# Performance work log

Hardware: AMD Instinct MI355X
Metric: run time of the kernel (lower is better)

The kernel has to match this reference:

```python
import jax, jax.numpy as jnp
import numpy as np

NEG_INF = -1e8  # masked_fill value from the torch code
EPS_DICE = 0.001
EPS_DIV = 1e-5
LOSS_FACTOR = 1.0  # loss['factor']


def conv2d(x, w, b, pad):
    # x: [B,C,H,W], w: [O,I,kh,kw] (OIHW), b: [O]
    y = jax.lax.conv_general_dilated(
        x, w, window_strides=(1, 1), padding=[(pad, pad), (pad, pad)],
        dimension_numbers=("NCHW", "OIHW", "NCHW"))
    return y + b[None, :, None, None]


def setup_inputs() -> dict:
    key = jax.random.key(0)
    ks = jax.random.split(key, 12)
    B, C, H, W = 2, 256, 64, 64
    s = 0.05  # small init scale to keep logits in a sane range
    inp = {
        "feats": jax.random.normal(ks[0], (B, C, H, W), jnp.float32),
        "masks": jax.random.randint(ks[1], (B, H, W), 0, 2).astype(jnp.float32),
        "layouts": jax.random.randint(ks[2], (B, H, W), 0, 16).astype(jnp.int32),
        "w_pre0": jax.random.normal(ks[3], (C, C, 3, 3), jnp.float32) * s,
        "b_pre0": jax.random.normal(ks[4], (C,), jnp.float32) * s,
        "w_pre1": jax.random.normal(ks[5], (C, C, 3, 3), jnp.float32) * s,
        "b_pre1": jax.random.normal(ks[6], (C,), jnp.float32) * s,
        "w_kernel": jax.random.normal(ks[7], (C + 1, C, 1, 1), jnp.float32) * s,
        "b_kernel": jax.random.normal(ks[8], (C + 1,), jnp.float32) * s,
        "w_feats": jax.random.normal(ks[9], (C, C, 1, 1), jnp.float32) * s,
        "b_feats": jax.random.normal(ks[10], (C,), jnp.float32) * s,
    }
    return inp


def reference(feats, masks, layouts, w_pre0, b_pre0, w_pre1, b_pre1,
              w_kernel, b_kernel, w_feats, b_feats):
    B, C, H, W = feats.shape
    # pre_kernel_convs: two 3x3 conv + ReLU
    h = jax.nn.relu(conv2d(feats, w_pre0, b_pre0, pad=1))
    h = jax.nn.relu(conv2d(h, w_pre1, b_pre1, pad=1))
    kernels = conv2d(h, w_kernel, b_kernel, pad=0)          # [B, C+1, H, W]
    f = conv2d(feats, w_feats, b_feats, pad=0)               # [B, C,   H, W]
    # permute(0,2,3,1).reshape(B, H*W, C+1): per-cell dynamic 1x1 conv params
    kernels = kernels.transpose(0, 2, 3, 1).reshape(B, H * W, C + 1)
    kw = kernels[..., :C]                                    # [B, P, C]
    kb = kernels[..., C]                                     # [B, P]
    # grouped 1x1 conv == batched matmul over channel dim
    logits = jnp.einsum("bpc,bchw->bphw", kw, f) + kb[:, :, None, None]
    logits = jnp.where(masks[:, None, :, :] > 0, logits, NEG_INF)  # [B,P,H,W]

    # --- training loss (dice, div='all') ---
    # segm_labels[b, r*W+c] = (layouts[b] == layouts[b,r,c])
    flat = layouts.reshape(B, H * W)
    labels = (layouts[:, None, :, :] == flat[:, :, None, None]).astype(logits.dtype)
    p = jax.nn.sigmoid(logits)
    d = 2.0 * (p * labels) / (p * p + EPS_DICE + labels * labels + EPS_DICE)
    loss_el = 1.0 - d                                        # [B, P, H, W]
    m_flat = masks.reshape(B, H * W)
    num = ((loss_el * masks[:, None, :, :]).sum((-1, -2)) * m_flat).sum(-1)  # [B]
    grid = masks.sum((1, 2))
    loss = (LOSS_FACTOR * num / (grid * grid + EPS_DIV)).mean()
    return logits, loss
```

## Files before the change

kernel.cpp:

```cpp
#include <hip/hip_runtime.h>
#include <hip/hip_bf16.h>
#include <math.h>

typedef __attribute__((ext_vector_type(8))) short bf16x8;
typedef __attribute__((ext_vector_type(4))) float f32x4;
typedef __hip_bfloat16 bf16_t;

#define NEG_INF_V -100000000.0f

__device__ __forceinline__ void gload16(const void* g, void* l) {
  __builtin_amdgcn_global_load_lds(
      (const __attribute__((address_space(1))) unsigned int*)g,
      (__attribute__((address_space(3))) unsigned int*)l, 16, 0, 0);
}

__device__ __forceinline__ bf16x8 swzread(const short* base, int r, int c) {
  return *(const bf16x8*)(base + ((r * 8 + (c ^ (r & 7))) << 3));
}

__global__ __launch_bounds__(256) void pad_cast_k(
    const float* __restrict__ feats, bf16_t* __restrict__ x_pad) {
  __shared__ float s[64][65];
  const int t = threadIdx.x;
  const int y = blockIdx.x, c0 = blockIdx.y * 64, b = blockIdx.z;
  const float* fb = feats + ((size_t)b * 256 + c0) * 4096 + y * 64;
  for (int i = t; i < 64 * 64; i += 256) {
    int ci = i >> 6, x = i & 63;
    s[ci][x] = fb[(size_t)ci * 4096 + x];
  }
  __syncthreads();
  bf16_t* xp = x_pad + (size_t)b * (66 * 66 * 256) + ((size_t)(y + 1) * 66 + 1) * 256 + c0;
  for (int i = t; i < 64 * 64; i += 256) {
    int x = i >> 6, ci = i & 63;
    xp[(size_t)x * 256 + ci] = __float2bfloat16(s[ci][x]);
  }
}

__global__ __launch_bounds__(256) void castw3_k(
    const float* __restrict__ w0, const float* __restrict__ w1,
    bf16_t* __restrict__ o0, bf16_t* __restrict__ o1) {
  const int co = blockIdx.x, t = threadIdx.x;
  const float* ws = blockIdx.y ? w1 : w0;
  bf16_t* wd = blockIdx.y ? o1 : o0;
#pragma unroll
  for (int k = 0; k < 9; ++k)
    wd[(size_t)co * 2304 + k * 256 + t] = __float2bfloat16(ws[((size_t)co * 256 + t) * 9 + k]);
}

__global__ __launch_bounds__(256) void castw1_k(
    const float* __restrict__ wk, const float* __restrict__ wf,
    bf16_t* __restrict__ ok, bf16_t* __restrict__ of) {
  int i = blockIdx.x * 256 + threadIdx.x;
  if (i < 257 * 256) ok[i] = __float2bfloat16(wk[i]);
  else { int j = i - 257 * 256; if (j < 256 * 256) of[j] = __float2bfloat16(wf[j]); }
}

__global__ __launch_bounds__(256) void conv3x3_mfma_k(
    const bf16_t* __restrict__ xpad, const bf16_t* __restrict__ wr,
    const float* __restrict__ bias, bf16_t* __restrict__ out,
    int out_row_stride, int out_base, long out_bstride) {
  __shared__ __align__(16) short ldsA[2][4096];
  __shared__ __align__(16) short ldsB[2][4096];
  const int t = threadIdx.x, w = t >> 6, lane = t & 63;
  const int y = blockIdx.x, co0 = blockIdx.y * 64, b = blockIdx.z;
  const bf16_t* xb = xpad + (size_t)b * (66 * 66 * 256);
  const int wm = w >> 1, wn = w & 1;
  f32x4 acc[2][2] = {};

  int ar[2], ac[2];
#pragma unroll
  for (int p = 0; p < 2; ++p) {
    int u = (p * 4 + w) * 64 + lane;
    ar[p] = u >> 3;
    ac[p] = ((u & 7) ^ ((u >> 3) & 7)) * 8;
  }
  const int fr = lane & 15, fc = lane >> 4;

  auto stage = [&](int ks, int buf) {
    int kpos = ks >> 2, cik = (ks & 3) * 64;
    int ky = (kpos * 11) >> 5, kx = kpos - 3 * ky;
#pragma unroll
    for (int p = 0; p < 2; ++p) {
      gload16(xb + ((size_t)(y + ky) * 66 + (ar[p] + kx)) * 256 + cik + ac[p],
              &ldsA[buf][(p * 4 + w) * 512]);
      gload16(wr + (size_t)(co0 + ar[p]) * 2304 + kpos * 256 + cik + ac[p],
              &ldsB[buf][(p * 4 + w) * 512]);
    }
  };
  auto compute = [&](int buf) {
#pragma unroll
    for (int kk = 0; kk < 2; ++kk) {
      bf16x8 af[2], bfr[2];
#pragma unroll
      for (int m = 0; m < 2; ++m) af[m] = swzread(ldsA[buf], wm * 32 + m * 16 + fr, kk * 4 + fc);
#pragma unroll
      for (int n = 0; n < 2; ++n) bfr[n] = swzread(ldsB[buf], wn * 32 + n * 16 + fr, kk * 4 + fc);
#pragma unroll
      for (int m = 0; m < 2; ++m)
#pragma unroll
        for (int n = 0; n < 2; ++n)
          acc[m][n] = __builtin_amdgcn_mfma_f32_16x16x32_bf16(af[m], bfr[n], acc[m][n], 0, 0, 0);
    }
  };

  stage(0, 0);
  __syncthreads();
  for (int ks = 0; ks < 35; ++ks) {
    stage(ks + 1, (ks + 1) & 1);
    compute(ks & 1);
    __syncthreads();
  }
  compute(1);

  bf16_t* ob = out + (size_t)b * out_bstride;
  float bv[2];
#pragma unroll
  for (int n = 0; n < 2; ++n) bv[n] = bias[co0 + wn * 32 + n * 16 + fr];
#pragma unroll
  for (int m = 0; m < 2; ++m)
#pragma unroll
    for (int r = 0; r < 4; ++r) {
      int x = wm * 32 + m * 16 + fc * 4 + r;
      size_t ra = (size_t)out_base + (size_t)y * out_row_stride + (size_t)x * 256 + co0 + wn * 32 + fr;
#pragma unroll
      for (int n = 0; n < 2; ++n) {
        float v = acc[m][n][r] + bv[n];
        ob[ra + n * 16] = __float2bfloat16(fmaxf(v, 0.f));
      }
    }
}

template <bool KER>
__global__ __launch_bounds__(256) void conv1x1_mfma_k(
    const bf16_t* __restrict__ in, const bf16_t* __restrict__ wt,
    const float* __restrict__ bias, bf16_t* __restrict__ outw,
    float* __restrict__ outkb, int A0, int AS, long in_bstride, int comax) {
  __shared__ __align__(16) short ldsA[2][4096];
  __shared__ __align__(16) short ldsB[2][4096];
  const int t = threadIdx.x, w = t >> 6, lane = t & 63;
  const int y = blockIdx.x, co0 = blockIdx.y * 64, b = blockIdx.z;
  const bf16_t* inb = in + (size_t)b * in_bstride;
  const int wm = w >> 1, wn = w & 1;
  f32x4 acc[2][2] = {};

  int ar[2], ac[2];
#pragma unroll
  for (int p = 0; p < 2; ++p) {
    int u = (p * 4 + w) * 64 + lane;
    ar[p] = u >> 3;
    ac[p] = ((u & 7) ^ ((u >> 3) & 7)) * 8;
  }
  const int fr = lane & 15, fc = lane >> 4;

  auto stage = [&](int ks, int buf) {
    int cik = ks * 64;
#pragma unroll
    for (int p = 0; p < 2; ++p) {
      gload16(inb + (size_t)A0 + (size_t)y * AS + (size_t)ar[p] * 256 + cik + ac[p],
              &ldsA[buf][(p * 4 + w) * 512]);
      gload16(wt + (size_t)min(co0 + ar[p], comax - 1) * 256 + cik + ac[p],
              &ldsB[buf][(p * 4 + w) * 512]);
    }
  };
  auto compute = [&](int buf) {
#pragma unroll
    for (int kk = 0; kk < 2; ++kk) {
      bf16x8 af[2], bfr[2];
#pragma unroll
      for (int m = 0; m < 2; ++m) af[m] = swzread(ldsA[buf], wm * 32 + m * 16 + fr, kk * 4 + fc);
#pragma unroll
      for (int n = 0; n < 2; ++n) bfr[n] = swzread(ldsB[buf], wn * 32 + n * 16 + fr, kk * 4 + fc);
#pragma unroll
      for (int m = 0; m < 2; ++m)
#pragma unroll
        for (int n = 0; n < 2; ++n)
          acc[m][n] = __builtin_amdgcn_mfma_f32_16x16x32_bf16(af[m], bfr[n], acc[m][n], 0, 0, 0);
    }
  };

  stage(0, 0);
  __syncthreads();
  for (int ks = 0; ks < 3; ++ks) {
    stage(ks + 1, (ks + 1) & 1);
    compute(ks & 1);
    __syncthreads();
  }
  compute(1);

#pragma unroll
  for (int m = 0; m < 2; ++m)
#pragma unroll
    for (int r = 0; r < 4; ++r) {
      int x = wm * 32 + m * 16 + fc * 4 + r;
      int prow = y * 64 + x;
#pragma unroll
      for (int n = 0; n < 2; ++n) {
        int co = co0 + wn * 32 + n * 16 + fr;
        float v = acc[m][n][r] + bias[min(co, comax - 1)];
        if (KER) {
          if (co < 256) outw[((size_t)b * 4096 + prow) * 256 + co] = __float2bfloat16(v);
          else if (co == 256) outkb[(size_t)b * 4096 + prow] = v;
        } else {
          outw[((size_t)b * 4096 + prow) * 256 + co] = __float2bfloat16(v);
        }
      }
    }
}

__global__ __launch_bounds__(256) void logits_mfma_k(
    const bf16_t* __restrict__ kwt, const float* __restrict__ kb,
    const bf16_t* __restrict__ fft, const float* __restrict__ masks,
    const int* __restrict__ layouts, float* __restrict__ out,
    float* __restrict__ partial) {
  __shared__ __align__(16) short ldsA[2][4096];
  __shared__ __align__(16) short ldsB[2][8192];
  const int t = threadIdx.x, w = t >> 6, lane = t & 63;
  const int p0 = blockIdx.x * 64, q0 = blockIdx.y * 128, b = blockIdx.z;
  const bf16_t* ab = kwt + (size_t)b * (4096 * 256);
  const bf16_t* bb = fft + (size_t)b * (4096 * 256);
  const int wm = w >> 1, wn = w & 1;
  f32x4 acc[2][4] = {};

  int ar[2], ac[2], br[4], bc[4];
#pragma unroll
  for (int p = 0; p < 2; ++p) {
    int u = (p * 4 + w) * 64 + lane;
    ar[p] = u >> 3;
    ac[p] = ((u & 7) ^ ((u >> 3) & 7)) * 8;
  }
#pragma unroll
  for (int p = 0; p < 4; ++p) {
    int u = (p * 4 + w) * 64 + lane;
    br[p] = u >> 3;
    bc[p] = ((u & 7) ^ ((u >> 3) & 7)) * 8;
  }
  const int fr = lane & 15, fc = lane >> 4;

  auto stage = [&](int ks, int buf) {
    int cik = ks * 64;
#pragma unroll
    for (int p = 0; p < 2; ++p)
      gload16(ab + (size_t)(p0 + ar[p]) * 256 + cik + ac[p], &ldsA[buf][(p * 4 + w) * 512]);
#pragma unroll
    for (int p = 0; p < 4; ++p)
      gload16(bb + (size_t)(q0 + br[p]) * 256 + cik + bc[p], &ldsB[buf][(p * 4 + w) * 512]);
  };
  auto compute = [&](int buf) {
#pragma unroll
    for (int kk = 0; kk < 2; ++kk) {
      bf16x8 af[2], bfr[4];
#pragma unroll
      for (int m = 0; m < 2; ++m) af[m] = swzread(ldsA[buf], wm * 32 + m * 16 + fr, kk * 4 + fc);
#pragma unroll
      for (int n = 0; n < 4; ++n) bfr[n] = swzread(ldsB[buf], wn * 64 + n * 16 + fr, kk * 4 + fc);
#pragma unroll
      for (int m = 0; m < 2; ++m)
#pragma unroll
        for (int n = 0; n < 4; ++n)
          acc[m][n] = __builtin_amdgcn_mfma_f32_16x16x32_bf16(af[m], bfr[n], acc[m][n], 0, 0, 0);
    }
  };

  stage(0, 0);
  __syncthreads();
  for (int ks = 0; ks < 3; ++ks) {
    stage(ks + 1, (ks + 1) & 1);
    compute(ks & 1);
    __syncthreads();
  }
  compute(1);

  float mq[4];
  int layq[4];
#pragma unroll
  for (int n = 0; n < 4; ++n) {
    int q = q0 + wn * 64 + n * 16 + fr;
    mq[n] = masks[b * 4096 + q];
    layq[n] = layouts[b * 4096 + q];
  }
  float sl[8];
#pragma unroll
  for (int i = 0; i < 8; ++i) sl[i] = 0.f;
  float* outb = out + (size_t)b * 4096 * 4096;
#pragma unroll
  for (int m = 0; m < 2; ++m) {
#pragma unroll
    for (int r = 0; r < 4; ++r) {
      int p = p0 + wm * 32 + m * 16 + fc * 4 + r;
      float kbv = kb[b * 4096 + p];
      int layp = layouts[b * 4096 + p];
      float s = 0.f;
      size_t ra = (size_t)p * 4096 + q0 + wn * 64 + fr;
#pragma unroll
      for (int n = 0; n < 4; ++n) {
        float lg = (mq[n] > 0.f) ? (acc[m][n][r] + kbv) : NEG_INF_V;
        outb[ra + n * 16] = lg;
        float pz = 1.f / (1.f + __expf(-lg));
        float lab = (layp == layq[n]) ? 1.f : 0.f;
        float d = 2.f * pz * lab / (pz * pz + lab + 0.002f);
        s += (1.f - d) * mq[n];
      }
      sl[m * 4 + r] = s;
    }
  }
#pragma unroll
  for (int i = 0; i < 8; ++i) {
    float v = sl[i];
    v += __shfl_xor(v, 1); v += __shfl_xor(v, 2);
    v += __shfl_xor(v, 4); v += __shfl_xor(v, 8);
    sl[i] = v;
  }
  if (fr == 0) {
    int qt = blockIdx.y * 2 + wn;
#pragma unroll
    for (int m = 0; m < 2; ++m)
#pragma unroll
      for (int r = 0; r < 4; ++r) {
        int p = p0 + wm * 32 + m * 16 + fc * 4 + r;
        partial[((size_t)b * 4096 + p) * 64 + qt] = sl[m * 4 + r];
      }
  }
}

__global__ __launch_bounds__(256) void rowsum_k(
    const float* __restrict__ partial, const float* __restrict__ masks,
    float* __restrict__ accum) {
  const int t = threadIdx.x, w = t >> 6, lane = t & 63;
  const int idx = blockIdx.x * 256 + t;
  const int b = idx >> 12;
  const float* pp = partial + (size_t)idx * 64;
  float s = 0.f;
#pragma unroll
  for (int k = 0; k < 64; ++k) s += pp[k];
  float mp = masks[idx];
  float num = s * mp;
#pragma unroll
  for (int off = 32; off; off >>= 1) {
    num += __shfl_down(num, off);
    mp += __shfl_down(mp, off);
  }
  __shared__ float sn[4], sm[4];
  if (lane == 0) { sn[w] = num; sm[w] = mp; }
  __syncthreads();
  if (t == 0) {
    atomicAdd(&accum[b * 2], sn[0] + sn[1] + sn[2] + sn[3]);
    atomicAdd(&accum[b * 2 + 1], sm[0] + sm[1] + sm[2] + sm[3]);
  }
}

__global__ void loss_final_k(const float* __restrict__ accum, float* __restrict__ out_loss) {
  if (threadIdx.x == 0) {
    float l0 = accum[0] / (accum[1] * accum[1] + 1e-5f);
    float l1 = accum[2] / (accum[3] * accum[3] + 1e-5f);
    out_loss[0] = 0.5f * (l0 + l1);
  }
}

extern "C" void kernel_launch(void* const* d_in, const int* in_sizes, int n_in,
                              void* d_out, int out_size, void* d_ws, size_t ws_size,
                              hipStream_t stream) {
  const float* feats = (const float*)d_in[0];
  const float* masks = (const float*)d_in[1];
  const int* layouts = (const int*)d_in[2];
  const float* w_pre0 = (const float*)d_in[3];
  const float* b_pre0 = (const float*)d_in[4];
  const float* w_pre1 = (const float*)d_in[5];
  const float* b_pre1 = (const float*)d_in[6];
  const float* w_kernel = (const float*)d_in[7];
  const float* b_kernel = (const float*)d_in[8];
  const float* w_feats = (const float*)d_in[9];
  const float* b_feats = (const float*)d_in[10];

  bf16_t* x_pad = (bf16_t*)d_ws;
  bf16_t* h1p = x_pad + 2 * 1115136;
  bf16_t* h2 = h1p + 2 * 1115136;
  bf16_t* w0r = h2 + 2 * 1048576;
  bf16_t* w1r = w0r + 589824;
  bf16_t* wkb = w1r + 589824;
  bf16_t* wfb = wkb + 65792;
  bf16_t* kwt = wfb + 65536;
  bf16_t* fft = kwt + 2 * 1048576;
  float* kb = (float*)(fft + 2 * 1048576);
  float* partial = kb + 8192;
  float* accum = partial + 524288;
  float* out = (float*)d_out;

  hipMemsetAsync(x_pad, 0, (size_t)4 * 1115136 * sizeof(bf16_t), stream);
  hipMemsetAsync(accum, 0, 4 * sizeof(float), stream);

  pad_cast_k<<<dim3(64, 4, 2), 256, 0, stream>>>(feats, x_pad);
  castw3_k<<<dim3(256, 2), 256, 0, stream>>>(w_pre0, w_pre1, w0r, w1r);
  castw1_k<<<dim3(514), 256, 0, stream>>>(w_kernel, w_feats, wkb, wfb);

  conv3x3_mfma_k<<<dim3(64, 4, 2), 256, 0, stream>>>(
      x_pad, w0r, b_pre0, h1p, 66 * 256, 67 * 256, 1115136L);
  conv3x3_mfma_k<<<dim3(64, 4, 2), 256, 0, stream>>>(
      h1p, w1r, b_pre1, h2, 64 * 256, 0, 1048576L);

  conv1x1_mfma_k<true><<<dim3(64, 5, 2), 256, 0, stream>>>(
      h2, wkb, b_kernel, kwt, kb, 0, 16384, 1048576L, 257);
  conv1x1_mfma_k<false><<<dim3(64, 4, 2), 256, 0, stream>>>(
      x_pad, wfb, b_feats, fft, nullptr, 67 * 256, 66 * 256, 1115136L, 256);

  logits_mfma_k<<<dim3(64, 32, 2), 256, 0, stream>>>(
      kwt, kb, fft, masks, layouts, out, partial);

  rowsum_k<<<dim3(32), 256, 0, stream>>>(partial, masks, accum);
  loss_final_k<<<1, 64, 0, stream>>>(accum, out + (size_t)2 * 4096 * 4096);
}
```

Measured before the change: 283.4 us.

## Enlarge logits tile, deepen K-steps, fuse weight casts and write padding in-kernel

The logits GEMM tile grows from 64x128 to 128x128 per block, giving each wave 4x4 MFMA accumulators and halving the grid. The 3x3 conv now stages 128 channels per K-step, cutting the step count and barriers. The 1x1 conv loads all of K=256 at once and drops its pipelining. Padding borders for x_pad are written inside pad_cast_k instead of by a full memset, and the two weight-cast kernels merge into one launch. More LDS and registers per block may lower occupancy.

Result: slower. 293.6 us (+3.6%).

```diff
diff --git a/kernel.cpp b/kernel.cpp
--- a/kernel.cpp
+++ b/kernel.cpp
@@ -23,78 +23,95 @@
   __shared__ float s[64][65];
   const int t = threadIdx.x;
   const int y = blockIdx.x, c0 = blockIdx.y * 64, b = blockIdx.z;
-  const float* fb = feats + ((size_t)b * 256 + c0) * 4096 + y * 64;
+  bf16_t* xp = x_pad + (size_t)b * (66 * 66 * 256) + (size_t)y * 66 * 256 + c0;
+  if (y == 0 || y == 65) {
+    for (int i = t; i < 66 * 64; i += 256) {
+      int px = i >> 6, ci = i & 63;
+      xp[(size_t)px * 256 + ci] = __float2bfloat16(0.f);
+    }
+    return;
+  }
+  const float* fb = feats + ((size_t)b * 256 + c0) * 4096 + (size_t)(y - 1) * 64;
   for (int i = t; i < 64 * 64; i += 256) {
     int ci = i >> 6, x = i & 63;
     s[ci][x] = fb[(size_t)ci * 4096 + x];
   }
   __syncthreads();
-  bf16_t* xp = x_pad + (size_t)b * (66 * 66 * 256) + ((size_t)(y + 1) * 66 + 1) * 256 + c0;
+  if (t < 128) {
+    int px = (t >> 6) * 65, ci = t & 63;
+    xp[(size_t)px * 256 + ci] = __float2bfloat16(0.f);
+  }
   for (int i = t; i < 64 * 64; i += 256) {
-    int x = i >> 6, ci = i & 63;
-    xp[(size_t)x * 256 + ci] = __float2bfloat16(s[ci][x]);
-  }
-}
-
-__global__ __launch_bounds__(256) void castw3_k(
+    int xi = i >> 6, ci = i & 63;
+    xp[(size_t)(xi + 1) * 256 + ci] = __float2bfloat16(s[ci][xi]);
+  }
+}
+
+__global__ __launch_bounds__(256) void castw_all_k(
     const float* __restrict__ w0, const float* __restrict__ w1,
-    bf16_t* __restrict__ o0, bf16_t* __restrict__ o1) {
-  const int co = blockIdx.x, t = threadIdx.x;
-  const float* ws = blockIdx.y ? w1 : w0;
-  bf16_t* wd = blockIdx.y ? o1 : o0;
-#pragma unroll
-  for (int k = 0; k < 9; ++k)
-    wd[(size_t)co * 2304 + k * 256 + t] = __float2bfloat16(ws[((size_t)co * 256 + t) * 9 + k]);
-}
-
-__global__ __launch_bounds__(256) void castw1_k(
     const float* __restrict__ wk, const float* __restrict__ wf,
+    bf16_t* __restrict__ o0, bf16_t* __restrict__ o1,
     bf16_t* __restrict__ ok, bf16_t* __restrict__ of) {
-  int i = blockIdx.x * 256 + threadIdx.x;
-  if (i < 257 * 256) ok[i] = __float2bfloat16(wk[i]);
-  else { int j = i - 257 * 256; if (j < 256 * 256) of[j] = __float2bfloat16(wf[j]); }
+  const int bid = blockIdx.x, t = threadIdx.x;
+  if (bid < 512) {
+    int which = bid >> 8, co = bid & 255;
+    const float* ws = which ? w1 : w0;
+    bf16_t* wd = which ? o1 : o0;
+#pragma unroll
+    for (int k = 0; k < 9; ++k)
+      wd[(size_t)co * 2304 + k * 256 + t] = __float2bfloat16(ws[((size_t)co * 256 + t) * 9 + k]);
+  } else {
+    int i = (bid - 512) * 256 + t;
+    if (i < 257 * 256) ok[i] = __float2bfloat16(wk[i]);
+    else { int j = i - 257 * 256; if (j < 256 * 256) of[j] = __float2bfloat16(wf[j]); }
+  }
 }
 
 __global__ __launch_bounds__(256) void conv3x3_mfma_k(
     const bf16_t* __restrict__ xpad, const bf16_t* __restrict__ wr,
     const float* __restrict__ bias, bf16_t* __restrict__ out,
     int out_row_stride, int out_base, long out_bstride) {
-  __shared__ __align__(16) short ldsA[2][4096];
-  __shared__ __align__(16) short ldsB[2][4096];
+  __shared__ __align__(16) short ldsA[2][8192];
+  __shared__ __align__(16) short ldsB[2][8192];
   const int t = threadIdx.x, w = t >> 6, lane = t & 63;
   const int y = blockIdx.x, co0 = blockIdx.y * 64, b = blockIdx.z;
   const bf16_t* xb = xpad + (size_t)b * (66 * 66 * 256);
   const int wm = w >> 1, wn = w & 1;
   f32x4 acc[2][2] = {};
 
-  int ar[2], ac[2];
-#pragma unroll
-  for (int p = 0; p < 2; ++p) {
-    int u = (p * 4 + w) * 64 + lane;
-    ar[p] = u >> 3;
-    ac[p] = ((u & 7) ^ ((u >> 3) & 7)) * 8;
+  int arow[4], akh[4], alsl[4];
+#pragma unroll
+  for (int pp = 0; pp < 4; ++pp) {
+    int u = (pp * 4 + w) * 64 + lane;
+    int gr = u >> 3, slot = u & 7;
+    arow[pp] = gr & 63; akh[pp] = gr >> 6;
+    alsl[pp] = (slot ^ (gr & 7)) * 8;
   }
   const int fr = lane & 15, fc = lane >> 4;
 
   auto stage = [&](int ks, int buf) {
-    int kpos = ks >> 2, cik = (ks & 3) * 64;
+    int kpos = ks >> 1, ck0 = (ks & 1) * 128;
     int ky = (kpos * 11) >> 5, kx = kpos - 3 * ky;
 #pragma unroll
-    for (int p = 0; p < 2; ++p) {
-      gload16(xb + ((size_t)(y + ky) * 66 + (ar[p] + kx)) * 256 + cik + ac[p],
-              &ldsA[buf][(p * 4 + w) * 512]);
-      gload16(wr + (size_t)(co0 + ar[p]) * 2304 + kpos * 256 + cik + ac[p],
-              &ldsB[buf][(p * 4 + w) * 512]);
+    for (int pp = 0; pp < 4; ++pp) {
+      gload16(xb + ((size_t)(y + ky) * 66 + arow[pp] + kx) * 256 + kpos * 0 + ck0 + akh[pp] * 64 + alsl[pp]
+                 + (size_t)kpos * 0,
+              &ldsA[buf][(pp * 4 + w) * 512]);
+      gload16(wr + (size_t)(co0 + arow[pp]) * 2304 + kpos * 256 + ck0 + akh[pp] * 64 + alsl[pp],
+              &ldsB[buf][(pp * 4 + w) * 512]);
     }
   };
   auto compute = [&](int buf) {
 #pragma unroll
-    for (int kk = 0; kk < 2; ++kk) {
+    for (int kk = 0; kk < 4; ++kk) {
+      const short* bA = &ldsA[buf][(kk >> 1) * 4096];
+      const short* bB = &ldsB[buf][(kk >> 1) * 4096];
+      int c = (kk & 1) * 4 + fc;
       bf16x8 af[2], bfr[2];
 #pragma unroll
-      for (int m = 0; m < 2; ++m) af[m] = swzread(ldsA[buf], wm * 32 + m * 16 + fr, kk * 4 + fc);
-#pragma unroll
-      for (int n = 0; n < 2; ++n) bfr[n] = swzread(ldsB[buf], wn * 32 + n * 16 + fr, kk * 4 + fc);
+      for (int m = 0; m < 2; ++m) af[m] = swzread(bA, wm * 32 + m * 16 + fr, c);
+#pragma unroll
+      for (int n = 0; n < 2; ++n) bfr[n] = swzread(bB, wn * 32 + n * 16 + fr, c);
 #pragma unroll
       for (int m = 0; m < 2; ++m)
 #pragma unroll
@@ -105,7 +122,7 @@
 
   stage(0, 0);
   __syncthreads();
-  for (int ks = 0; ks < 35; ++ks) {
+  for (int ks = 0; ks < 17; ++ks) {
     stage(ks + 1, (ks + 1) & 1);
     compute(ks & 1);
     __syncthreads();
@@ -135,57 +152,43 @@
     const bf16_t* __restrict__ in, const bf16_t* __restrict__ wt,
     const float* __restrict__ bias, bf16_t* __restrict__ outw,
     float* __restrict__ outkb, int A0, int AS, long in_bstride, int comax) {
-  __shared__ __align__(16) short ldsA[2][4096];
-  __shared__ __align__(16) short ldsB[2][4096];
+  __shared__ __align__(16) short ldsA[16384];
+  __shared__ __align__(16) short ldsB[16384];
   const int t = threadIdx.x, w = t >> 6, lane = t & 63;
   const int y = blockIdx.x, co0 = blockIdx.y * 64, b = blockIdx.z;
   const bf16_t* inb = in + (size_t)b * in_bstride;
   const int wm = w >> 1, wn = w & 1;
   f32x4 acc[2][2] = {};
-
-  int ar[2], ac[2];
-#pragma unroll
-  for (int p = 0; p < 2; ++p) {
-    int u = (p * 4 + w) * 64 + lane;
-    ar[p] = u >> 3;
-    ac[p] = ((u & 7) ^ ((u >> 3) & 7)) * 8;
-  }
   const int fr = lane & 15, fc = lane >> 4;
 
-  auto stage = [&](int ks, int buf) {
-    int cik = ks * 64;
-#pragma unroll
-    for (int p = 0; p < 2; ++p) {
-      gload16(inb + (size_t)A0 + (size_t)y * AS + (size_t)ar[p] * 256 + cik + ac[p],
-              &ldsA[buf][(p * 4 + w) * 512]);
-      gload16(wt + (size_t)min(co0 + ar[p], comax - 1) * 256 + cik + ac[p],
-              &ldsB[buf][(p * 4 + w) * 512]);
-    }
-  };
-  auto compute = [&](int buf) {
-#pragma unroll
-    for (int kk = 0; kk < 2; ++kk) {
-      bf16x8 af[2], bfr[2];
-#pragma unroll
-      for (int m = 0; m < 2; ++m) af[m] = swzread(ldsA[buf], wm * 32 + m * 16 + fr, kk * 4 + fc);
-#pragma unroll
-      for (int n = 0; n < 2; ++n) bfr[n] = swzread(ldsB[buf], wn * 32 + n * 16 + fr, kk * 4 + fc);
-#pragma unroll
-      for (int m = 0; m < 2; ++m)
-#pragma unroll
-        for (int n = 0; n < 2; ++n)
-          acc[m][n] = __builtin_amdgcn_mfma_f32_16x16x32_bf16(af[m], bfr[n], acc[m][n], 0, 0, 0);
-    }
-  };
-
-  stage(0, 0);
+#pragma unroll
+  for (int pp = 0; pp < 8; ++pp) {
+    int u = (pp * 4 + w) * 64 + lane;
+    int gr = u >> 3, slot = u & 7;
+    int row = gr & 63, kh = gr >> 6;
+    int lsl = (slot ^ (gr & 7)) * 8;
+    gload16(inb + (size_t)A0 + (size_t)y * AS + (size_t)row * 256 + kh * 64 + lsl,
+            &ldsA[(pp * 4 + w) * 512]);
+    gload16(wt + (size_t)min(co0 + row, comax - 1) * 256 + kh * 64 + lsl,
+            &ldsB[(pp * 4 + w) * 512]);
+  }
   __syncthreads();
-  for (int ks = 0; ks < 3; ++ks) {
-    stage(ks + 1, (ks + 1) & 1);
-    compute(ks & 1);
-    __syncthreads();
-  }
-  compute(1);
+#pragma unroll
+  for (int kk = 0; kk < 8; ++kk) {
+    const short* bA = &ldsA[(kk >> 1) * 4096];
+    const short* bB = &ldsB[(kk >> 1) * 4096];
+    int c = (kk & 1) * 4 + fc;
+    bf16x8 af[2], bfr[2];
+#pragma unroll
+    for (int m = 0; m < 2; ++m) af[m] = swzread(bA, wm * 32 + m * 16 + fr, c);
+#pragma unroll
+    for (int n = 0; n < 2; ++n) bfr[n] = swzread(bB, wn * 32 + n * 16 + fr, c);
+#pragma unroll
+    for (int m = 0; m < 2; ++m)
+#pragma unroll
+      for (int n = 0; n < 2; ++n)
+        acc[m][n] = __builtin_amdgcn_mfma_f32_16x16x32_bf16(af[m], bfr[n], acc[m][n], 0, 0, 0);
+  }
 
 #pragma unroll
   for (int m = 0; m < 2; ++m)
@@ -212,49 +215,44 @@
     const bf16_t* __restrict__ fft, const float* __restrict__ masks,
     const int* __restrict__ layouts, float* __restrict__ out,
     float* __restrict__ partial) {
-  __shared__ __align__(16) short ldsA[2][4096];
+  __shared__ __align__(16) short ldsA[2][8192];
   __shared__ __align__(16) short ldsB[2][8192];
   const int t = threadIdx.x, w = t >> 6, lane = t & 63;
-  const int p0 = blockIdx.x * 64, q0 = blockIdx.y * 128, b = blockIdx.z;
+  const int p0 = blockIdx.x * 128, q0 = blockIdx.y * 128, b = blockIdx.z;
   const bf16_t* ab = kwt + (size_t)b * (4096 * 256);
   const bf16_t* bb = fft + (size_t)b * (4096 * 256);
   const int wm = w >> 1, wn = w & 1;
-  f32x4 acc[2][4] = {};
-
-  int ar[2], ac[2], br[4], bc[4];
-#pragma unroll
-  for (int p = 0; p < 2; ++p) {
-    int u = (p * 4 + w) * 64 + lane;
-    ar[p] = u >> 3;
-    ac[p] = ((u & 7) ^ ((u >> 3) & 7)) * 8;
-  }
-#pragma unroll
-  for (int p = 0; p < 4; ++p) {
-    int u = (p * 4 + w) * 64 + lane;
-    br[p] = u >> 3;
-    bc[p] = ((u & 7) ^ ((u >> 3) & 7)) * 8;
+  f32x4 acc[4][4] = {};
+
+  int grow[4], glsl[4];
+#pragma unroll
+  for (int pp = 0; pp < 4; ++pp) {
+    int u = (pp * 4 + w) * 64 + lane;
+    int gr = u >> 3, slot = u & 7;
+    grow[pp] = gr;
+    glsl[pp] = (slot ^ (gr & 7)) * 8;
   }
   const int fr = lane & 15, fc = lane >> 4;
 
   auto stage = [&](int ks, int buf) {
     int cik = ks * 64;
 #pragma unroll
-    for (int p = 0; p < 2; ++p)
-      gload16(ab + (size_t)(p0 + ar[p]) * 256 + cik + ac[p], &ldsA[buf][(p * 4 + w) * 512]);
-#pragma unroll
-    for (int p = 0; p < 4; ++p)
-      gload16(bb + (size_t)(q0 + br[p]) * 256 + cik + bc[p], &ldsB[buf][(p * 4 + w) * 512]);
+    for (int pp = 0; pp < 4; ++pp) {
+      gload16(ab + (size_t)(p0 + grow[pp]) * 256 + cik + glsl[pp], &ldsA[buf][(pp * 4 + w) * 512]);
+      gload16(bb + (size_t)(q0 + grow[pp]) * 256 + cik + glsl[pp], &ldsB[buf][(pp * 4 + w) * 512]);
+    }
   };
   auto compute = [&](int buf) {
 #pragma unroll
     for (int kk = 0; kk < 2; ++kk) {
-      bf16x8 af[2], bfr[4];
-#pragma unroll
-      for (int m = 0; m < 2; ++m) af[m] = swzread(ldsA[buf], wm * 32 + m * 16 + fr, kk * 4 + fc);
-#pragma unroll
-      for (int n = 0; n < 4; ++n) bfr[n] = swzread(ldsB[buf], wn * 64 + n * 16 + fr, kk * 4 + fc);
-#pragma unroll
-      for (int m = 0; m < 2; ++m)
+      int c = kk * 4 + fc;
+      bf16x8 af[4], bfr[4];
+#pragma unroll
+      for (int m = 0; m < 4; ++m) af[m] = swzread(ldsA[buf], wm * 64 + m * 16 + fr, c);
+#pragma unroll
+      for (int n = 0; n < 4; ++n) bfr[n] = swzread(ldsB[buf], wn * 64 + n * 16 + fr, c);
+#pragma unroll
+      for (int m = 0; m < 4; ++m)
 #pragma unroll
         for (int n = 0; n < 4; ++n)
           acc[m][n] = __builtin_amdgcn_mfma_f32_16x16x32_bf16(af[m], bfr[n], acc[m][n], 0, 0, 0);
@@ -278,15 +276,15 @@
     mq[n] = masks[b * 4096 + q];
     layq[n] = layouts[b * 4096 + q];
   }
-  float sl[8];
-#pragma unroll
-  for (int i = 0; i < 8; ++i) sl[i] = 0.f;
+  float sl[16];
+#pragma unroll
+  for (int i = 0; i < 16; ++i) sl[i] = 0.f;
   float* outb = out + (size_t)b * 4096 * 4096;
 #pragma unroll
-  for (int m = 0; m < 2; ++m) {
+  for (int m = 0; m < 4; ++m) {
 #pragma unroll
     for (int r = 0; r < 4; ++r) {
-      int p = p0 + wm * 32 + m * 16 + fc * 4 + r;
+      int p = p0 + wm * 64 + m * 16 + fc * 4 + r;
       float kbv = kb[b * 4096 + p];
       int layp = layouts[b * 4096 + p];
       float s = 0.f;
@@ -304,7 +302,7 @@
     }
   }
 #pragma unroll
-  for (int i = 0; i < 8; ++i) {
+  for (int i = 0; i < 16; ++i) {
     float v = sl[i];
     v += __shfl_xor(v, 1); v += __shfl_xor(v, 2);
     v += __shfl_xor(v, 4); v += __shfl_xor(v, 8);
@@ -313,10 +311,10 @@
   if (fr == 0) {
     int qt = blockIdx.y * 2 + wn;
 #pragma unroll
-    for (int m = 0; m < 2; ++m)
+    for (int m = 0; m < 4; ++m)
 #pragma unroll
       for (int r = 0; r < 4; ++r) {
-        int p = p0 + wm * 32 + m * 16 + fc * 4 + r;
+        int p = p0 + wm * 64 + m * 16 + fc * 4 + r;
         partial[((size_t)b * 4096 + p) * 64 + qt] = sl[m * 4 + r];
       }
   }
@@ -385,12 +383,12 @@
   float* accum = partial + 524288;
   float* out = (float*)d_out;
 
-  hipMemsetAsync(x_pad, 0, (size_t)4 * 1115136 * sizeof(bf16_t), stream);
+  hipMemsetAsync(h1p, 0, (size_t)2 * 1115136 * sizeof(bf16_t), stream);
   hipMemsetAsync(accum, 0, 4 * sizeof(float), stream);
 
-  pad_cast_k<<<dim3(64, 4, 2), 256, 0, stream>>>(feats, x_pad);
-  castw3_k<<<dim3(256, 2), 256, 0, stream>>>(w_pre0, w_pre1, w0r, w1r);
-  castw1_k<<<dim3(514), 256, 0, stream>>>(w_kernel, w_feats, wkb, wfb);
+  pad_cast_k<<<dim3(66, 4, 2), 256, 0, stream>>>(feats, x_pad);
+  castw_all_k<<<dim3(1026), 256, 0, stream>>>(w_pre0, w_pre1, w_kernel, w_feats,
+                                              w0r, w1r, wkb, wfb);
 
   conv3x3_mfma_k<<<dim3(64, 4, 2), 256, 0, stream>>>(
       x_pad, w0r, b_pre0, h1p, 66 * 256, 67 * 256, 1115136L);
@@ -402,7 +400,7 @@
   conv1x1_mfma_k<false><<<dim3(64, 4, 2), 256, 0, stream>>>(
       x_pad, wfb, b_feats, fft, nullptr, 67 * 256, 66 * 256, 1115136L, 256);
 
-  logits_mfma_k<<<dim3(64, 32, 2), 256, 0, stream>>>(
+  logits_mfma_k<<<dim3(32, 32, 2), 256, 0, stream>>>(
       kwt, kb, fft, masks, layouts, out, partial);
 
   rowsum_k<<<dim3(32), 256, 0, stream>>>(partial, masks, accum);
```
